# Optimization experiments

Hardware: AMD Instinct MI355X
Metric: run time of the kernel (lower is better)

Reference implementation:

```python
import jax, jax.numpy as jnp
import numpy as np


def setup_inputs() -> dict:
    key = jax.random.key(0)
    k1, k2 = jax.random.split(key)
    b, c, n = 16, 64, 65536
    features = jax.random.normal(k1, (b, c, n), dtype=jnp.float32)
    coords = jax.random.normal(k2, (b, 3, n), dtype=jnp.float32)  # roughly in [-1,1], clamp handles outliers
    return {"features": features, "coords": coords, "resolution": 32}


def reference(features, coords, resolution):
    r = int(resolution)
    r2, r3 = r * r, r * r * r
    b, c, n = features.shape
    # scale_pvcnn path: map coords from [-1,1] to voxel space, clamp, round
    norm_coords = jnp.clip(((coords + 1.0) / 2.0) * r, 0.0, r - 1)
    vox_coords = jnp.round(norm_coords).astype(jnp.int32)
    # linear voxel index per point: [b, n]
    indices = vox_coords[:, 0] * r2 + vox_coords[:, 1] * r + vox_coords[:, 2]
    # append ones channel for counting
    feat1 = jnp.concatenate(
        [features, jnp.ones((b, 1, n), dtype=features.dtype)], axis=1
    )  # [b, c+1, n]

    def scatter_one(f, idx):  # f: [c+1, n], idx: [n]
        return jnp.zeros((c + 1, r3), dtype=f.dtype).at[:, idx].add(f)

    out = jax.vmap(scatter_one)(feat1, indices)  # [b, c+1, r^3]
    cnt = out[:, -1:, :]
    cnt = jnp.where(cnt == 0, jnp.asarray(1e-5, cnt.dtype), cnt)
    vox_feature = (out[:, :-1, :] / cnt).reshape(b, c, r, r, r)
    return vox_feature, norm_coords
```

## Files before the change

kernel.cpp:

```cpp
#include <hip/hip_runtime.h>

constexpr int Rr = 32;
constexpr int R2 = Rr * Rr;
constexpr int R3 = Rr * Rr * Rr;
constexpr int Bb = 16;
constexpr int Cc = 64;
constexpr int Nn = 65536;
constexpr int VOX_ELEMS = Bb * Cc * R3;
constexpr int NCELL = Bb * R3;

__device__ __forceinline__ unsigned pack_bf16(float a, float b)
{
    unsigned ua = __float_as_uint(a);
    unsigned ub = __float_as_uint(b);
    ua += 0x7FFFu + ((ua >> 16) & 1u);
    ub += 0x7FFFu + ((ub >> 16) & 1u);
    return (ua >> 16) | (ub & 0xFFFF0000u);
}

__global__ __launch_bounds__(256) void zero_cnt_kernel(float4* __restrict__ base)
{
    int i = blockIdx.x * 256 + threadIdx.x;
    base[i] = float4{0.0f, 0.0f, 0.0f, 0.0f};
}

__global__ __launch_bounds__(256) void vox_coords_kernel(
    const float* __restrict__ coords,
    float* __restrict__ norm_out,
    int* __restrict__ idx_out,
    int* __restrict__ cnt)
{
    int t = blockIdx.x * 256 + threadIdx.x;
    int b = t >> 16;
    int i = t & (Nn - 1);

    const float* cp = coords + (size_t)b * 3 * Nn + i;
    float x = cp[0];
    float y = cp[Nn];
    float z = cp[2 * Nn];

    float nx = fminf(fmaxf((x + 1.0f) * 16.0f, 0.0f), 31.0f);
    float ny = fminf(fmaxf((y + 1.0f) * 16.0f, 0.0f), 31.0f);
    float nz = fminf(fmaxf((z + 1.0f) * 16.0f, 0.0f), 31.0f);

    float* np_ = norm_out + (size_t)b * 3 * Nn + i;
    np_[0]      = nx;
    np_[Nn]     = ny;
    np_[2 * Nn] = nz;

    int idx = (int)rintf(nx) * R2 + (int)rintf(ny) * Rr + (int)rintf(nz);

    int k = atomicAdd(&cnt[(b << 15) + idx], 1);
    idx_out[t] = (idx << 3) | min(k, 7);
}

__global__ __launch_bounds__(256) void slot3zero_kernel(
    const int* __restrict__ cnt, unsigned short* __restrict__ voxT4)
{
    int g = blockIdx.x * 256 + threadIdx.x;
    int cell = g >> 3;
    int p    = g & 7;
    if (cnt[cell] > 4)
        *(float4*)(voxT4 + ((size_t)cell << 8) + 192 + (p << 3)) =
            float4{0.0f, 0.0f, 0.0f, 0.0f};
}

__global__ __launch_bounds__(256) void tscatter_store_kernel(
    const float* __restrict__ feat,
    const int* __restrict__ idx_ws,
    const int* __restrict__ cnt,
    unsigned short* __restrict__ voxT4)
{
    __shared__ float lds[64 * 65];
    __shared__ int   dest_sm[64];
    __shared__ int   at_sm[64];
    int b    = blockIdx.x >> 10;
    int tile = blockIdx.x & 1023;
    int n0   = tile << 6;
    int t    = threadIdx.x;

    if (t < 64) {
        int e    = idx_ws[(b << 16) + n0 + t];
        int cell = (b << 15) + (e >> 3);
        int k    = e & 7;
        int cn   = cnt[cell];
        dest_sm[t] = (cell << 8) + (min(k, 3) << 6);
        at_sm[t]   = (k >= 3 && cn > 4) ? 1 : 0;
    }

#pragma unroll
    for (int q = 0; q < 4; ++q) {
        int c  = (t >> 4) + (q << 4);
        int n4 = (t & 15) << 2;
        float4 v = *(const float4*)(feat + (((size_t)(b * Cc + c)) << 16) + n0 + n4);
        lds[(n4 + 0) * 65 + c] = v.x;
        lds[(n4 + 1) * 65 + c] = v.y;
        lds[(n4 + 2) * 65 + c] = v.z;
        lds[(n4 + 3) * 65 + c] = v.w;
    }
    __syncthreads();

    int wave = t >> 6, lane = t & 63;
    int hi = lane >> 5;
    int m  = lane & 31;
#pragma unroll
    for (int kk = 0; kk < 8; ++kk) {
        int n = (wave << 4) + (kk << 1) + hi;
        float f0 = lds[n * 65 + (m << 1) + 0];
        float f1 = lds[n * 65 + (m << 1) + 1];
        unsigned pk = pack_bf16(f0, f1);
        unsigned short* addr = voxT4 + (size_t)dest_sm[n] + (m << 1);
        if (at_sm[n]) {
            asm volatile("global_atomic_pk_add_bf16 %0, %1, off"
                         :: "v"(addr), "v"(pk) : "memory");
        } else {
            *(unsigned*)addr = pk;
        }
    }
}

__global__ __launch_bounds__(256) void merge_transpose_kernel(
    const unsigned short* __restrict__ voxT4,
    const int* __restrict__ cnt,
    float* __restrict__ vox)
{
    __shared__ float lds[64 * 65];
    int b    = blockIdx.x >> 9;
    int tile = blockIdx.x & 511;
    int v0   = tile << 6;
    int t    = threadIdx.x;
    int cl   = t >> 2;
    int q    = t & 3;

    int cell = (b << 15) + v0 + cl;
    int cn   = cnt[cell];
    int kmax = min(cn, 4);

    float acc[16];
#pragma unroll
    for (int j = 0; j < 16; ++j) acc[j] = 0.0f;

    const unsigned short* base = voxT4 + ((size_t)cell << 8) + (q << 4);
    for (int k = 0; k < kmax; ++k) {
        uint4 w0 = *(const uint4*)(base + (k << 6));
        uint4 w1 = *(const uint4*)(base + (k << 6) + 8);
        const unsigned* w = &w0.x;
#pragma unroll
        for (int j = 0; j < 4; ++j) {
            acc[2 * j + 0] += __uint_as_float(w[j] << 16);
            acc[2 * j + 1] += __uint_as_float(w[j] & 0xFFFF0000u);
        }
        const unsigned* w2 = &w1.x;
#pragma unroll
        for (int j = 0; j < 4; ++j) {
            acc[8 + 2 * j + 0] += __uint_as_float(w2[j] << 16);
            acc[8 + 2 * j + 1] += __uint_as_float(w2[j] & 0xFFFF0000u);
        }
    }

    float inv = cn ? 1.0f / (float)cn : 0.0f;
#pragma unroll
    for (int j = 0; j < 16; ++j)
        lds[cl * 65 + (q << 4) + j] = acc[j] * inv;
    __syncthreads();

    int wave = t >> 6, lane = t & 63;
#pragma unroll
    for (int k = 0; k < 16; ++k) {
        int c = (wave << 4) + k;
        vox[(((size_t)(b * Cc + c)) << 15) + v0 + lane] = lds[lane * 65 + c];
    }
}

extern "C" void kernel_launch(void* const* d_in, const int* in_sizes, int n_in,
                              void* d_out, int out_size, void* d_ws, size_t ws_size,
                              hipStream_t stream)
{
    const float* features = (const float*)d_in[0];
    const float* coords   = (const float*)d_in[1];

    float* out      = (float*)d_out;
    float* vox      = out;
    float* norm_out = out + VOX_ELEMS;

    char* ws = (char*)d_ws;
    int*            cnt    = (int*)ws;            ws += (size_t)NCELL * 4;
    int*            idx_ws = (int*)ws;            ws += (size_t)Bb * Nn * 4;
    unsigned short* voxT4  = (unsigned short*)ws;

    zero_cnt_kernel<<<NCELL * 4 / 16 / 256, 256, 0, stream>>>((float4*)cnt);
    vox_coords_kernel<<<(Bb * Nn) / 256, 256, 0, stream>>>(coords, norm_out, idx_ws, cnt);
    slot3zero_kernel<<<NCELL * 8 / 256, 256, 0, stream>>>(cnt, voxT4);
    tscatter_store_kernel<<<Bb * 1024, 256, 0, stream>>>(features, idx_ws, cnt, voxT4);
    merge_transpose_kernel<<<Bb * 512, 256, 0, stream>>>(voxT4, cnt, vox);
}
```

Baseline: 224.7 us.

## Process scatter and merge in batch chunks to keep staging buffer cache-resident

Splits the slot-zero, transposed scatter, and merge kernels into a loop over groups of 4 batches, using a per-chunk staging buffer indexed by local cell. This shrinks the bf16 staging footprint so that data written by the scatter may still sit in the last-level cache when the merge reads it, which should cut HBM traffic. In exchange there are more kernel launches and smaller grids per launch, so the GPU may be less fully occupied and launch gaps add up.

After: 260.6 us. 16.0% more time.

```diff
diff --git a/kernel.cpp b/kernel.cpp
--- a/kernel.cpp
+++ b/kernel.cpp
@@ -8,6 +8,7 @@
 constexpr int Nn = 65536;
 constexpr int VOX_ELEMS = Bb * Cc * R3;
 constexpr int NCELL = Bb * R3;
+constexpr int CB = 4;
 
 __device__ __forceinline__ unsigned pack_bf16(float a, float b)
 {
@@ -55,13 +56,13 @@
 }
 
 __global__ __launch_bounds__(256) void slot3zero_kernel(
-    const int* __restrict__ cnt, unsigned short* __restrict__ voxT4)
+    const int* __restrict__ cnt, unsigned short* __restrict__ voxT4, int b0)
 {
     int g = blockIdx.x * 256 + threadIdx.x;
-    int cell = g >> 3;
-    int p    = g & 7;
-    if (cnt[cell] > 4)
-        *(float4*)(voxT4 + ((size_t)cell << 8) + 192 + (p << 3)) =
+    int cellLoc = g >> 3;
+    int p       = g & 7;
+    if (cnt[(b0 << 15) + cellLoc] > 4)
+        *(float4*)(voxT4 + ((size_t)cellLoc << 8) + 192 + (p << 3)) =
             float4{0.0f, 0.0f, 0.0f, 0.0f};
 }
 
@@ -69,22 +70,24 @@
     const float* __restrict__ feat,
     const int* __restrict__ idx_ws,
     const int* __restrict__ cnt,
-    unsigned short* __restrict__ voxT4)
+    unsigned short* __restrict__ voxT4,
+    int b0)
 {
     __shared__ float lds[64 * 65];
     __shared__ int   dest_sm[64];
     __shared__ int   at_sm[64];
-    int b    = blockIdx.x >> 10;
+    int bb   = blockIdx.x >> 10;
+    int b    = b0 + bb;
     int tile = blockIdx.x & 1023;
     int n0   = tile << 6;
     int t    = threadIdx.x;
 
     if (t < 64) {
-        int e    = idx_ws[(b << 16) + n0 + t];
-        int cell = (b << 15) + (e >> 3);
-        int k    = e & 7;
-        int cn   = cnt[cell];
-        dest_sm[t] = (cell << 8) + (min(k, 3) << 6);
+        int e       = idx_ws[(b << 16) + n0 + t];
+        int cellLoc = (bb << 15) + (e >> 3);
+        int k       = e & 7;
+        int cn      = cnt[(b << 15) + (e >> 3)];
+        dest_sm[t] = (cellLoc << 8) + (min(k, 3) << 6);
         at_sm[t]   = (k >= 3 && cn > 4) ? 1 : 0;
     }
 
@@ -122,25 +125,27 @@
 __global__ __launch_bounds__(256) void merge_transpose_kernel(
     const unsigned short* __restrict__ voxT4,
     const int* __restrict__ cnt,
-    float* __restrict__ vox)
+    float* __restrict__ vox,
+    int b0)
 {
     __shared__ float lds[64 * 65];
-    int b    = blockIdx.x >> 9;
+    int bb   = blockIdx.x >> 9;
+    int b    = b0 + bb;
     int tile = blockIdx.x & 511;
     int v0   = tile << 6;
     int t    = threadIdx.x;
     int cl   = t >> 2;
     int q    = t & 3;
 
-    int cell = (b << 15) + v0 + cl;
-    int cn   = cnt[cell];
-    int kmax = min(cn, 4);
+    int cellLoc = (bb << 15) + v0 + cl;
+    int cn      = cnt[(b << 15) + v0 + cl];
+    int kmax    = min(cn, 4);
 
     float acc[16];
 #pragma unroll
     for (int j = 0; j < 16; ++j) acc[j] = 0.0f;
 
-    const unsigned short* base = voxT4 + ((size_t)cell << 8) + (q << 4);
+    const unsigned short* base = voxT4 + ((size_t)cellLoc << 8) + (q << 4);
     for (int k = 0; k < kmax; ++k) {
         uint4 w0 = *(const uint4*)(base + (k << 6));
         uint4 w1 = *(const uint4*)(base + (k << 6) + 8);
@@ -190,7 +195,10 @@
 
     zero_cnt_kernel<<<NCELL * 4 / 16 / 256, 256, 0, stream>>>((float4*)cnt);
     vox_coords_kernel<<<(Bb * Nn) / 256, 256, 0, stream>>>(coords, norm_out, idx_ws, cnt);
-    slot3zero_kernel<<<NCELL * 8 / 256, 256, 0, stream>>>(cnt, voxT4);
-    tscatter_store_kernel<<<Bb * 1024, 256, 0, stream>>>(features, idx_ws, cnt, voxT4);
-    merge_transpose_kernel<<<Bb * 512, 256, 0, stream>>>(voxT4, cnt, vox);
-}
+
+    for (int b0 = 0; b0 < Bb; b0 += CB) {
+        slot3zero_kernel<<<CB * R3 * 8 / 256, 256, 0, stream>>>(cnt, voxT4, b0);
+        tscatter_store_kernel<<<CB * 1024, 256, 0, stream>>>(features, idx_ws, cnt, voxT4, b0);
+        merge_transpose_kernel<<<CB * 512, 256, 0, stream>>>(voxT4, cnt, vox, b0);
+    }
+}
```
